# Kernel optimization log

Measured on AMD Instinct MI355X. Metric: run time of the kernel, lower is better.

Reference implementation:

```python
import jax, jax.numpy as jnp
import numpy as np

HBV_LO = jnp.array([1.0, 50.0, 0.05, 0.01, 0.001, 0.2, 0.0, 0.0, -2.5, 0.5, 0.0, 0.0, 0.3, 0.0], dtype=jnp.float32)
HBV_HI = jnp.array([6.0, 1000.0, 0.9, 0.5, 0.2, 1.0, 10.0, 100.0, 2.5, 10.0, 0.1, 0.2, 5.0, 1.0], dtype=jnp.float32)
TDLST = (1, 13)  # 1-based indices of dynamic parameters (BETA, BETAET)
PRECS = 1e-5


def setup_inputs() -> dict:
    key = jax.random.key(0)
    k1, k2 = jax.random.split(key)
    Nstep, Ngrid, mu = 365, 1000, 16
    x = jax.random.uniform(k1, (Nstep, Ngrid, 3), dtype=jnp.float32)  # [P, T, ETpot]
    parameters = jax.random.uniform(k2, (Nstep, Ngrid, 14, mu), dtype=jnp.float32)
    return {"x": x, "parameters": parameters, "staind": Nstep - 1}


def _hbv_run(x, parameters, staind):
    mu = parameters.shape[-1]
    Nstep, Ngrid, _ = x.shape
    # scale raw [0,1] params to physical ranges: [Nstep, Ngrid, 14, mu]
    parAllTrans = HBV_LO[None, None, :, None] + parameters * (HBV_HI - HBV_LO)[None, None, :, None]
    # dynamic params (tdlst) vary per timestep; others frozen at timestep staind
    dynmask = jnp.zeros((14,), jnp.float32).at[jnp.array([ix - 1 for ix in TDLST])].set(1.0)
    m = dynmask[None, None, :, None]
    parFull = parAllTrans * m + parAllTrans[staind][None] * (1.0 - m)

    s0 = jnp.full((Ngrid, mu), 0.001, dtype=jnp.float32)
    init = (s0, s0, s0, s0, s0)  # SNOWPACK, MELTWATER, SM, SUZ, SLZ

    def step(state, xs):
        SP, MW, SM, SUZ, SLZ = state
        Pv, Tv, Ev, par = xs
        P = Pv[:, None]
        T = Tv[:, None]
        ETp = Ev[:, None]
        BETA, FC, K0, K1, K2, LP, PERCp, UZL, TT, CFMAX, CFR, CWH, BETAET, C = [par[:, i, :] for i in range(14)]
        RAIN = P * (T >= TT).astype(jnp.float32)
        SNOW = P * (T < TT).astype(jnp.float32)
        SP = SP + SNOW
        melt = jnp.minimum(jnp.maximum(CFMAX * (T - TT), 0.0), SP)
        MW = MW + melt
        SP = SP - melt
        refr = jnp.minimum(jnp.maximum(CFR * CFMAX * (TT - T), 0.0), MW)
        SP = SP + refr
        MW = MW - refr
        tosoil = jnp.maximum(MW - CWH * SP, 0.0)
        MW = MW - tosoil
        wet = jnp.clip((SM / FC) ** BETA, 0.0, 1.0)
        recharge = (RAIN + tosoil) * wet
        excess = jnp.maximum(SM - FC, 0.0)
        SM = SM - excess
        evapf = jnp.clip((SM / (LP * FC)) ** BETAET, 0.0, 1.0)
        ETact = jnp.minimum(SM, ETp * evapf)
        SM = jnp.maximum(SM - ETact, PRECS)
        SM = SM + RAIN + tosoil - recharge
        cap = jnp.minimum(SLZ, C * SLZ * (1.0 - jnp.minimum(SM / FC, 1.0)))
        SM = jnp.maximum(SM + cap, PRECS)
        SLZ = jnp.maximum(SLZ - cap, PRECS)
        SUZ = SUZ + recharge + excess
        PERC = jnp.minimum(SUZ, PERCp)
        SUZ = SUZ - PERC
        Q0 = K0 * jnp.maximum(SUZ - UZL, 0.0)
        SUZ = SUZ - Q0
        Q1 = K1 * SUZ
        SUZ = SUZ - Q1
        SLZ = SLZ + PERC
        Q2 = K2 * SLZ
        SLZ = SLZ - Q2
        return (SP, MW, SM, SUZ, SLZ), Q0 + Q1 + Q2

    xs = (x[:, :, 0], x[:, :, 1], x[:, :, 2], parFull)
    _, Qsimmu = jax.lax.scan(step, init, xs)  # [Nstep, Ngrid, mu]
    return Qsimmu.mean(-1)[:, :, None]  # muwts=None, routOpt=False -> [Nstep, Ngrid, 1]


def reference(x, parameters, staind):
    return _hbv_run(x, parameters, staind)
```

## Files before the change

### kernel.cpp

```cpp
#include <hip/hip_runtime.h>


static constexpr int   NSTEP = 365;
static constexpr int   NGRID = 1000;
static constexpr int   MU    = 16;
static constexpr float PRECS = 1e-5f;
static constexpr int   DEPTH = 10;

__device__ __forceinline__ float fast_pow(float xx, float yy) {
    return __builtin_amdgcn_exp2f(yy * __builtin_amdgcn_logf(xx));
}

template <int CTRL>
__device__ __forceinline__ float dpp_add(float v) {
    int r = __builtin_amdgcn_update_dpp(0, __float_as_int(v), CTRL, 0xF, 0xF, true);
    return v + __int_as_float(r);
}

__global__ __launch_bounds__(64)
void hbv_kernel(const float* __restrict__ x,
                const float* __restrict__ par,
                const int*   __restrict__ staind_p,
                float*       __restrict__ out)
{
    __shared__ float qlds[NSTEP * 4];

    const int lane = threadIdx.x;
    const int m    = lane & 15;
    const int gl   = lane >> 4;
    const int g    = blockIdx.x * 4 + gl;
    const int staind = *staind_p;

    const size_t tstride = (size_t)NGRID * 14 * MU;
    const int    xstride = NGRID * 3;

    const float* ps = par + (size_t)staind * tstride + (size_t)g * 14 * MU + m;
    const float FC    = 50.0f  + ps[ 1*MU] * (1000.0f - 50.0f);
    const float K0    = 0.05f  + ps[ 2*MU] * (0.9f  - 0.05f);
    const float K1    = 0.01f  + ps[ 3*MU] * (0.5f  - 0.01f);
    const float K2    = 0.001f + ps[ 4*MU] * (0.2f  - 0.001f);
    const float LP    = 0.2f   + ps[ 5*MU] * (1.0f  - 0.2f);
    const float PERCp =          ps[ 6*MU] * 10.0f;
    const float UZL   =          ps[ 7*MU] * 100.0f;
    const float TT    = -2.5f  + ps[ 8*MU] * 5.0f;
    const float CFMAX = 0.5f   + ps[ 9*MU] * (10.0f - 0.5f);
    const float CFR   =          ps[10*MU] * 0.1f;
    const float CWH   =          ps[11*MU] * 0.2f;
    const float C     =          ps[13*MU] * 1.0f;

    const float rFC   = 1.0f / FC;
    const float rLPFC = 1.0f / (LP * FC);
    const float CRF   = CFR * CFMAX;

    float SP = 1e-3f, MW = 1e-3f, SM = 1e-3f, SUZ = 1e-3f, SLZ = 1e-3f;

    auto step = [&](int t, float P, float T, float E, float p0, float p12) {
        const float BETA   = 1.0f + p0  * 5.0f;
        const float BETAET = 0.3f + p12 * 4.7f;
        const float RAIN = (T >= TT) ? P : 0.0f;
        const float SNOW = P - RAIN;
        const float dT   = T - TT;
        const float acap = fmaxf(CFMAX * dT, 0.0f);
        const float bcap = fmaxf(CRF * (-dT), 0.0f);

        const float SP1  = SP + SNOW;
        const float melt = fminf(acap, SP1);
        const float SP2  = SP1 - melt;
        const float MW1  = MW + melt;
        const float refr = fminf(bcap, MW1);
        const float MW2  = MW1 - refr;
        const float SP3  = SP2 + refr;
        const float lim  = CWH * SP3;
        const float tosoil = fmaxf(MW2 - lim, 0.0f);
        SP = SP3;
        MW = fminf(MW2, lim);

        const float wet    = fminf(fast_pow(SM * rFC, BETA), 1.0f);
        const float excess = fmaxf(SM - FC, 0.0f);
        const float SM1    = fminf(SM, FC);
        const float evapf  = fminf(fast_pow(SM1 * rLPFC, BETAET), 1.0f);
        const float SM2    = fmaxf(SM1 - E * evapf, PRECS);
        const float rt     = RAIN + tosoil;
        const float recharge = rt * wet;
        const float SM3    = SM2 + rt - recharge;
        const float CSLZ   = C * SLZ;
        const float cap    = fminf(SLZ, CSLZ * (1.0f - fminf(SM3 * rFC, 1.0f)));
        SM = fmaxf(SM3 + cap, PRECS);
        const float SLZ1   = fmaxf(SLZ - cap, PRECS);

        const float SUZ1 = SUZ + recharge + excess;
        const float PERC = fminf(SUZ1, PERCp);
        const float SUZ2 = SUZ1 - PERC;
        const float w0   = fmaxf(SUZ2 - UZL, 0.0f);
        const float Q0   = K0 * w0;
        const float SUZ3 = SUZ2 - Q0;
        const float Q1   = K1 * SUZ3;
        SUZ = SUZ3 - Q1;
        const float SLZ2 = SLZ1 + PERC;
        const float Q2   = K2 * SLZ2;
        SLZ = SLZ2 - Q2;

        float Q = Q0 + Q1 + Q2;
        Q = dpp_add<0xB1>(Q);
        Q = dpp_add<0x4E>(Q);
        Q = dpp_add<0x141>(Q);
        Q = dpp_add<0x140>(Q);
        qlds[t * 4 + gl] = Q * 0.0625f;
    };

    const float* pd = par + (size_t)g * 14 * MU + m;
    const float* xp = x   + (size_t)g * 3;

    float bP[DEPTH], bT[DEPTH], bE[DEPTH], b0[DEPTH], b12[DEPTH];
    const float* pdp = pd;
    const float* xpp = xp;
#pragma unroll
    for (int j = 0; j < DEPTH; ++j) {
        b0[j]  = pdp[0];
        b12[j] = pdp[12*MU];
        bP[j]  = xpp[0];
        bT[j]  = xpp[1];
        bE[j]  = xpp[2];
        pdp += tstride;
        xpp += xstride;
    }

    for (int tb = 0; tb < 350; tb += DEPTH) {
#pragma unroll
        for (int j = 0; j < DEPTH; ++j) {
            const float P = bP[j], T = bT[j], E = bE[j], p0 = b0[j], p12 = b12[j];
            b0[j]  = pdp[0];
            b12[j] = pdp[12*MU];
            bP[j]  = xpp[0];
            bT[j]  = xpp[1];
            bE[j]  = xpp[2];
            pdp += tstride;
            xpp += xstride;
            step(tb + j, P, T, E, p0, p12);
        }
    }

#pragma unroll
    for (int j = 0; j < DEPTH; ++j) {
        const float P = bP[j], T = bT[j], E = bE[j], p0 = b0[j], p12 = b12[j];
        b0[j]  = pdp[0];
        b12[j] = pdp[12*MU];
        bP[j]  = xpp[0];
        bT[j]  = xpp[1];
        bE[j]  = xpp[2];
        if (j < 4) { pdp += tstride; xpp += xstride; }
        step(350 + j, P, T, E, p0, p12);
    }

#pragma unroll
    for (int j = 0; j < 5; ++j)
        step(360 + j, bP[j], bT[j], bE[j], b0[j], b12[j]);

    const int gbase = blockIdx.x * 4;
    for (int i = lane; i < NSTEP * 4; i += 64) {
        const int t  = i >> 2;
        const int gg = i & 3;
        out[t * NGRID + gbase + gg] = qlds[i];
    }
}

extern "C" void kernel_launch(void* const* d_in, const int* in_sizes, int n_in,
                              void* d_out, int out_size, void* d_ws, size_t ws_size,
                              hipStream_t stream) {
    const float* x      = (const float*)d_in[0];
    const float* par    = (const float*)d_in[1];
    const int*   staind = (const int*)d_in[2];
    float*       out    = (float*)d_out;

    hipLaunchKernelGGL(hbv_kernel, dim3(NGRID / 4), dim3(64), 0, stream,
                       x, par, staind, out);
}
```

Measured before the change: 65.47 us.

## Defer mu-reduction to epilogue and fold pow constants into log space

```diff
diff --git a/kernel.cpp b/kernel.cpp
--- a/kernel.cpp
+++ b/kernel.cpp
@@ -6,16 +6,7 @@
 static constexpr int   MU    = 16;
 static constexpr float PRECS = 1e-5f;
 static constexpr int   DEPTH = 10;
-
-__device__ __forceinline__ float fast_pow(float xx, float yy) {
-    return __builtin_amdgcn_exp2f(yy * __builtin_amdgcn_logf(xx));
-}
-
-template <int CTRL>
-__device__ __forceinline__ float dpp_add(float v) {
-    int r = __builtin_amdgcn_update_dpp(0, __float_as_int(v), CTRL, 0xF, 0xF, true);
-    return v + __int_as_float(r);
-}
+static constexpr int   QPAD  = 68;
 
 __global__ __launch_bounds__(64)
 void hbv_kernel(const float* __restrict__ x,
@@ -23,12 +14,13 @@
                 const int*   __restrict__ staind_p,
                 float*       __restrict__ out)
 {
-    __shared__ float qlds[NSTEP * 4];
+    __shared__ float qlds[NSTEP * QPAD];
 
     const int lane = threadIdx.x;
     const int m    = lane & 15;
     const int gl   = lane >> 4;
-    const int g    = blockIdx.x * 4 + gl;
+    const int gbase = blockIdx.x * 4;
+    const int g    = gbase + gl;
     const int staind = *staind_p;
 
     const size_t tstride = (size_t)NGRID * 14 * MU;
@@ -44,19 +36,20 @@
     const float UZL   =          ps[ 7*MU] * 100.0f;
     const float TT    = -2.5f  + ps[ 8*MU] * 5.0f;
     const float CFMAX = 0.5f   + ps[ 9*MU] * (10.0f - 0.5f);
-    const float CFR   =          ps[10*MU] * 0.1f;
+    const float CRF   =          ps[10*MU] * 0.1f * CFMAX;
     const float CWH   =          ps[11*MU] * 0.2f;
     const float C     =          ps[13*MU] * 1.0f;
-
     const float rFC   = 1.0f / FC;
-    const float rLPFC = 1.0f / (LP * FC);
-    const float CRF   = CFR * CFMAX;
+    const float lgFC   = __builtin_amdgcn_logf(FC);
+    const float lgLPFC = __builtin_amdgcn_logf(LP * FC);
 
     float SP = 1e-3f, MW = 1e-3f, SM = 1e-3f, SUZ = 1e-3f, SLZ = 1e-3f;
 
     auto step = [&](int t, float P, float T, float E, float p0, float p12) {
-        const float BETA   = 1.0f + p0  * 5.0f;
-        const float BETAET = 0.3f + p12 * 4.7f;
+        const float BETA    = 1.0f + p0  * 5.0f;
+        const float BETAET  = 0.3f + p12 * 4.7f;
+        const float nBlgFC  = -BETA   * lgFC;
+        const float nBElgLP = -BETAET * lgLPFC;
         const float RAIN = (T >= TT) ? P : 0.0f;
         const float SNOW = P - RAIN;
         const float dT   = T - TT;
@@ -75,24 +68,25 @@
         SP = SP3;
         MW = fminf(MW2, lim);
 
-        const float wet    = fminf(fast_pow(SM * rFC, BETA), 1.0f);
+        const float lg    = __builtin_amdgcn_logf(SM);
+        const float wet   = __builtin_amdgcn_exp2f(fminf(fmaf(BETA, lg, nBlgFC), 0.0f));
         const float excess = fmaxf(SM - FC, 0.0f);
-        const float SM1    = fminf(SM, FC);
-        const float evapf  = fminf(fast_pow(SM1 * rLPFC, BETAET), 1.0f);
-        const float SM2    = fmaxf(SM1 - E * evapf, PRECS);
-        const float rt     = RAIN + tosoil;
+        const float SM1   = fminf(SM, FC);
+        const float lg1   = fminf(lg, lgFC);
+        const float evapf = __builtin_amdgcn_exp2f(fminf(fmaf(BETAET, lg1, nBElgLP), 0.0f));
+        const float SM2   = fmaxf(fmaf(-E, evapf, SM1), PRECS);
+        const float rt    = RAIN + tosoil;
         const float recharge = rt * wet;
-        const float SM3    = SM2 + rt - recharge;
-        const float CSLZ   = C * SLZ;
-        const float cap    = fminf(SLZ, CSLZ * (1.0f - fminf(SM3 * rFC, 1.0f)));
+        const float SM3   = SM2 + rt - recharge;
+        const float capf  = fmaxf(fmaf(-SM3, rFC, 1.0f), 0.0f);
+        const float cap   = fminf(SLZ, (C * SLZ) * capf);
         SM = fmaxf(SM3 + cap, PRECS);
-        const float SLZ1   = fmaxf(SLZ - cap, PRECS);
+        const float SLZ1  = fmaxf(SLZ - cap, PRECS);
 
         const float SUZ1 = SUZ + recharge + excess;
         const float PERC = fminf(SUZ1, PERCp);
         const float SUZ2 = SUZ1 - PERC;
-        const float w0   = fmaxf(SUZ2 - UZL, 0.0f);
-        const float Q0   = K0 * w0;
+        const float Q0   = K0 * fmaxf(SUZ2 - UZL, 0.0f);
         const float SUZ3 = SUZ2 - Q0;
         const float Q1   = K1 * SUZ3;
         SUZ = SUZ3 - Q1;
@@ -100,12 +94,7 @@
         const float Q2   = K2 * SLZ2;
         SLZ = SLZ2 - Q2;
 
-        float Q = Q0 + Q1 + Q2;
-        Q = dpp_add<0xB1>(Q);
-        Q = dpp_add<0x4E>(Q);
-        Q = dpp_add<0x141>(Q);
-        Q = dpp_add<0x140>(Q);
-        qlds[t * 4 + gl] = Q * 0.0625f;
+        qlds[t * QPAD + lane] = Q0 + Q1 + Q2;
     };
 
     const float* pd = par + (size_t)g * 14 * MU + m;
@@ -156,11 +145,14 @@
     for (int j = 0; j < 5; ++j)
         step(360 + j, bP[j], bT[j], bE[j], b0[j], b12[j]);
 
-    const int gbase = blockIdx.x * 4;
     for (int i = lane; i < NSTEP * 4; i += 64) {
         const int t  = i >> 2;
         const int gg = i & 3;
-        out[t * NGRID + gbase + gg] = qlds[i];
+        const float* row = &qlds[t * QPAD + gg * 16];
+        float s = 0.0f;
+#pragma unroll
+        for (int k = 0; k < 16; ++k) s += row[k];
+        out[t * NGRID + gbase + gg] = s * 0.0625f;
     }
 }
 
```

Result: faster. 62.74 us (-4.2%).
